# Kernel tuning notes

Measured on AMD Instinct MI355X. Metric: run time of the kernel, lower is better.

Reference implementation:

```python
import jax, jax.numpy as jnp
import numpy as np

D = 128
H = 256


def setup_inputs() -> dict:
    key = jax.random.key(0)
    ks = jax.random.split(key, 16)
    B, T = 512, 128
    C = D + H + D  # combined = [x, h, mask]
    stdv_c = 1.0 / np.sqrt(C)
    stdv_d = 1.0 / np.sqrt(D)
    stdv_h = 1.0 / np.sqrt(H)
    u = lambda k, shape, s: jax.random.uniform(k, shape, jnp.float32, -s, s)
    return {
        "input": jax.random.normal(ks[0], (B, 4, T, D), jnp.float32),
        "X_mean": jax.random.normal(ks[1], (1, T, D), jnp.float32),
        "zl_w": u(ks[2], (H, C), stdv_c), "zl_b": u(ks[3], (H,), stdv_c),
        "rl_w": u(ks[4], (H, C), stdv_c), "rl_b": u(ks[5], (H,), stdv_c),
        "hl_w": u(ks[6], (H, C), stdv_c), "hl_b": u(ks[7], (H,), stdv_c),
        "gx_w": u(ks[8], (D, D), stdv_d), "gx_b": u(ks[9], (D,), stdv_d),
        "gh_w": u(ks[10], (H, D), stdv_d), "gh_b": u(ks[11], (H,), stdv_d),
        "fc_w": u(ks[12], (1, H), stdv_h), "fc_b": u(ks[13], (1,), stdv_h),
    }


def reference(input, X_mean, zl_w, zl_b, rl_w, rl_b, hl_w, hl_b,
              gx_w, gx_b, gh_w, gh_b, fc_w, fc_b):
    B = input.shape[0]
    # FilterLinear with identity filter: weight is masked to its diagonal
    gx_w_masked = gx_w * jnp.eye(D, dtype=gx_w.dtype)
    gx_diag = jnp.diagonal(gx_w_masked)  # elementwise equivalent

    # split channels and move time to leading axis for scan: [T, B, D]
    X = jnp.moveaxis(input[:, 0], 1, 0)
    X_last = jnp.moveaxis(input[:, 1], 1, 0)
    Mask = jnp.moveaxis(input[:, 2], 1, 0)
    Delta = jnp.moveaxis(input[:, 3], 1, 0)
    Xm = jnp.moveaxis(X_mean, 1, 0)  # [T, 1, D], broadcasts over batch

    h0 = jnp.zeros((B, H), jnp.float32)

    def step(h, inp):
        x, x_last, x_mean, m, d = inp
        delta_x = jnp.exp(-jax.nn.relu(d * gx_diag + gx_b))          # [B, D]
        delta_h = jnp.exp(-jax.nn.relu(d @ gh_w.T + gh_b))           # [B, H]
        x = m * x + (1 - m) * (delta_x * x_last + (1 - delta_x) * x_mean)
        h = delta_h * h
        combined = jnp.concatenate([x, h, m], axis=1)                # [B, D+H+D]
        z = jax.nn.sigmoid(combined @ zl_w.T + zl_b)
        r = jax.nn.sigmoid(combined @ rl_w.T + rl_b)
        combined_r = jnp.concatenate([x, r * h, m], axis=1)
        h_tilde = jnp.tanh(combined_r @ hl_w.T + hl_b)
        h = (1 - z) * h + z * h_tilde
        return h, h

    _, hs = jax.lax.scan(step, h0, (X, X_last, Xm, Mask, Delta))     # [T, B, H]
    outputs = jnp.moveaxis(hs, 0, 1)                                 # [B, T, H]
    # num_class == 2, output_last == False: binary head on all steps
    out = jax.nn.sigmoid(outputs @ fc_w.T + fc_b)                    # [B, T, 1]
    return out.astype(jnp.float32)
```

## Files before the change

kernel.cpp:

```cpp
#include <hip/hip_runtime.h>
#include <hip/hip_bf16.h>
#include <cstdint>

typedef unsigned int u32;
typedef unsigned short u16;
typedef __attribute__((ext_vector_type(8))) short bf16x8;
typedef __attribute__((ext_vector_type(4))) float f32x4;

#define TT 128
#define BB 512
#define DD 128
#define HH 256
#define CC 512

#define HDA_OFF 32768
#define PA_OFF  34816

#define BAR() do { asm volatile("s_waitcnt lgkmcnt(0)" ::: "memory"); \
                   __builtin_amdgcn_s_barrier(); \
                   asm volatile("" ::: "memory"); } while(0)

__device__ __forceinline__ u16 f2bf(float f){
  u32 u = __builtin_bit_cast(u32, f);
  u += 0x7FFFu + ((u >> 16) & 1u);
  return (u16)(u >> 16);
}
__device__ __forceinline__ float bflo(u32 w){ return __builtin_bit_cast(float, w << 16); }
__device__ __forceinline__ float bfhi(u32 w){ return __builtin_bit_cast(float, w & 0xFFFF0000u); }
__device__ __forceinline__ float bf1(u16 w){ return __builtin_bit_cast(float, ((u32)w) << 16); }
__device__ __forceinline__ float sigm(float x){ return 1.f / (1.f + __expf(-x)); }
__device__ __forceinline__ float tanh_fast(float x){
  float t = __expf(-2.f * fabsf(x));
  float r = (1.f - t) / (1.f + t);
  return copysignf(r, x);
}

__global__ __launch_bounds__(256) void prep_weights(
    const float* __restrict__ zl_w, const float* __restrict__ rl_w,
    const float* __restrict__ hl_w, const float* __restrict__ gh_w,
    const float* __restrict__ gx_w,
    u32* __restrict__ zlB, u32* __restrict__ rlB, u32* __restrict__ hlF,
    u32* __restrict__ Bpre, u32* __restrict__ ghF, float* __restrict__ gxd){
  int gid = blockIdx.x * 256 + threadIdx.x;
  if (gid < 32768){
    int d   = gid & 3;
    int l   = (gid >> 2) & 63;
    int kt  = (gid >> 8) & 7;
    int ntg = (gid >> 11) & 15;
    int nn  = 16*ntg + (l & 15);
    int kk  = 32*kt + 8*(l >> 4) + 2*d;
    int c0 = 128 + kk;
    zlB[gid] = (u32)f2bf(zl_w[nn*CC + c0]) | ((u32)f2bf(zl_w[nn*CC + c0 + 1]) << 16);
    rlB[gid] = (u32)f2bf(rl_w[nn*CC + c0]) | ((u32)f2bf(rl_w[nn*CC + c0 + 1]) << 16);
    hlF[gid] = (u32)f2bf(hl_w[nn*CC + c0]) | ((u32)f2bf(hl_w[nn*CC + c0 + 1]) << 16);
  }
  #pragma unroll
  for (int q = 0; q < 2; ++q){
    int id = q*65536 + gid;
    if (id < 98304){
      int d2 = id & 3;
      int l  = (id >> 2) & 63;
      int kt = (id >> 8) & 7;
      int nt = id >> 11;
      int g  = nt >> 4;
      int nc = (nt & 15)*16 + (l & 15);
      int k  = 32*kt + 8*(l >> 4) + 2*d2;
      int sc = (k < 128) ? k : k + 256;
      const float* W = (g == 0) ? zl_w : ((g == 1) ? rl_w : hl_w);
      Bpre[id] = (u32)f2bf(W[nc*CC + sc]) | ((u32)f2bf(W[nc*CC + sc + 1]) << 16);
    }
  }
  if (gid < 16384){
    int d2 = gid & 3;
    int l  = (gid >> 2) & 63;
    int kt = (gid >> 8) & 3;
    int nt = gid >> 10;
    int nc = nt*16 + (l & 15);
    int k  = 32*kt + 8*(l >> 4) + 2*d2;
    ghF[gid] = (u32)f2bf(gh_w[nc*DD + k]) | ((u32)f2bf(gh_w[nc*DD + k + 1]) << 16);
  }
  if (gid < 128) gxd[gid] = gx_w[gid*DD + gid];
}

__global__ __launch_bounds__(512, 2) void precompute_mfma(
    const float* __restrict__ input, const float* __restrict__ xmean,
    const float* __restrict__ gxd, const float* __restrict__ gx_b,
    const float* __restrict__ zl_b, const float* __restrict__ rl_b,
    const float* __restrict__ hl_b, const float* __restrict__ gh_b,
    const u32* __restrict__ Bpre, const u32* __restrict__ ghF,
    u32* __restrict__ zrp, float* __restrict__ hpre, float* __restrict__ dh){
  __shared__ __align__(16) u16 A1[4][8][64][8];
  __shared__ __align__(16) u16 A2[4][4][64][8];
  const int tid = threadIdx.x;
  const int r0 = blockIdx.x * 64;
  const int t  = r0 >> 9;
  const int b0 = r0 & 511;
  {
    int row = tid >> 3, dsg = tid & 7, d0 = dsg * 16;
    int b = b0 + row;
    const size_t ib = ((size_t)b * 4 * TT + t) * DD;
    int mt = row >> 4;
    #pragma unroll
    for (int gg = 0; gg < 2; ++gg){
      int db = d0 + 8*gg;
      float xv[8], lv[8], mv[8], dv[8], xm[8], gd[8], gb[8];
      #pragma unroll
      for (int q = 0; q < 2; ++q){
        *(float4*)&xv[q*4] = *(const float4*)&input[ib + 0*TT*DD + db + q*4];
        *(float4*)&lv[q*4] = *(const float4*)&input[ib + 1*TT*DD + db + q*4];
        *(float4*)&mv[q*4] = *(const float4*)&input[ib + 2*TT*DD + db + q*4];
        *(float4*)&dv[q*4] = *(const float4*)&input[ib + 3*TT*DD + db + q*4];
        *(float4*)&xm[q*4] = *(const float4*)&xmean[t*DD + db + q*4];
        *(float4*)&gd[q*4] = *(const float4*)&gxd[db + q*4];
        *(float4*)&gb[q*4] = *(const float4*)&gx_b[db + q*4];
      }
      union { u16 s[8]; bf16x8 v; } pe, pm, pd;
      #pragma unroll
      for (int j = 0; j < 8; ++j){
        float dxv = __expf(-fmaxf(dv[j]*gd[j] + gb[j], 0.f));
        float xe  = mv[j]*xv[j] + (1.f - mv[j])*(dxv*lv[j] + (1.f - dxv)*xm[j]);
        pe.s[j] = f2bf(xe);
        pm.s[j] = f2bf(mv[j]);
        pd.s[j] = f2bf(dv[j]);
      }
      int kt1 = db >> 5;
      int l1  = (row & 15) + 16*((db >> 3) & 3);
      *(bf16x8*)&A1[mt][kt1][l1][0]     = pe.v;
      *(bf16x8*)&A1[mt][4 + kt1][l1][0] = pm.v;
      *(bf16x8*)&A2[mt][kt1][l1][0]     = pd.v;
    }
  }
  __syncthreads();
  const int l = tid & 63, w = tid >> 6;
  const int wm = w >> 2, wn = w & 3;
  const int rowl = 4 * (l >> 4), coll = l & 15;
  f32x4 acc[2][12];
  #pragma unroll
  for (int m = 0; m < 2; ++m)
    #pragma unroll
    for (int i = 0; i < 12; ++i) acc[m][i] = (f32x4){0.f,0.f,0.f,0.f};
  #pragma unroll
  for (int kt = 0; kt < 8; ++kt){
    bf16x8 a0 = *(const bf16x8*)&A1[wm*2 + 0][kt][l][0];
    bf16x8 a1 = *(const bf16x8*)&A1[wm*2 + 1][kt][l][0];
    #pragma unroll
    for (int i = 0; i < 12; ++i){
      int nt = 4*i + wn;
      bf16x8 bf = *(const bf16x8*)(Bpre + ((nt*8 + kt)*64 + l)*4);
      acc[0][i] = __builtin_amdgcn_mfma_f32_16x16x32_bf16(a0, bf, acc[0][i], 0, 0, 0);
      acc[1][i] = __builtin_amdgcn_mfma_f32_16x16x32_bf16(a1, bf, acc[1][i], 0, 0, 0);
    }
  }
  #pragma unroll
  for (int m = 0; m < 2; ++m){
    int grow = r0 + wm*32 + m*16 + rowl;
    #pragma unroll
    for (int i = 0; i < 4; ++i){
      int lc = (4*i + wn)*16 + coll;
      float bz = zl_b[lc], br = rl_b[lc];
      #pragma unroll
      for (int rg = 0; rg < 4; ++rg){
        u32 pk = (u32)f2bf(acc[m][i][rg] + bz) | ((u32)f2bf(acc[m][i+4][rg] + br) << 16);
        zrp[(size_t)(grow + rg)*HH + lc] = pk;
      }
    }
    #pragma unroll
    for (int i = 8; i < 12; ++i){
      int lc = (4*(i-8) + wn)*16 + coll;
      float bh = hl_b[lc];
      #pragma unroll
      for (int rg = 0; rg < 4; ++rg)
        hpre[(size_t)(grow + rg)*HH + lc] = acc[m][i][rg] + bh;
    }
  }
  f32x4 ac2[2][4];
  #pragma unroll
  for (int m = 0; m < 2; ++m)
    #pragma unroll
    for (int i = 0; i < 4; ++i) ac2[m][i] = (f32x4){0.f,0.f,0.f,0.f};
  #pragma unroll
  for (int kt = 0; kt < 4; ++kt){
    bf16x8 a0 = *(const bf16x8*)&A2[wm*2 + 0][kt][l][0];
    bf16x8 a1 = *(const bf16x8*)&A2[wm*2 + 1][kt][l][0];
    #pragma unroll
    for (int i = 0; i < 4; ++i){
      int nt = wn*4 + i;
      bf16x8 bf = *(const bf16x8*)(ghF + ((nt*4 + kt)*64 + l)*4);
      ac2[0][i] = __builtin_amdgcn_mfma_f32_16x16x32_bf16(a0, bf, ac2[0][i], 0, 0, 0);
      ac2[1][i] = __builtin_amdgcn_mfma_f32_16x16x32_bf16(a1, bf, ac2[1][i], 0, 0, 0);
    }
  }
  #pragma unroll
  for (int m = 0; m < 2; ++m){
    int grow = r0 + wm*32 + m*16 + rowl;
    #pragma unroll
    for (int i = 0; i < 4; ++i){
      int lc = (wn*4 + i)*16 + coll;
      float bias = gh_b[lc];
      #pragma unroll
      for (int rg = 0; rg < 4; ++rg)
        dh[(size_t)(grow + rg)*HH + lc] = __expf(-fmaxf(ac2[m][i][rg] + bias, 0.f));
    }
  }
}

__global__ __launch_bounds__(512, 2) void recurrent_mfma(
    const u32* __restrict__ zrp, const float* __restrict__ hpre,
    const float* __restrict__ dh,
    const u32* __restrict__ zlB, const u32* __restrict__ rlB,
    const u32* __restrict__ hlF, u16* __restrict__ hout){
  __shared__ u32 smem[36864];
  const int tid = threadIdx.x;
  const int l = tid & 63, w = tid >> 6;
  const int b0 = blockIdx.x * 16;
  const int rowb = 4 * (l >> 4);
  const int col0 = 32*w + (l & 15);

  #pragma unroll
  for (int i = 0; i < 64; ++i) smem[i*512 + tid] = hlF[i*512 + tid];
  #pragma unroll
  for (int i = 0; i < 4; ++i) smem[HDA_OFF + i*512 + tid] = 0;

  bf16x8 zb[2][8], rb[2][8];
  #pragma unroll
  for (int nt = 0; nt < 2; ++nt){
    #pragma unroll
    for (int kt = 0; kt < 8; ++kt){
      int off = (((w*2 + nt)*8 + kt)*64 + l)*4;
      zb[nt][kt] = *(const bf16x8*)(zlB + off);
      rb[nt][kt] = *(const bf16x8*)(rlB + off);
    }
  }
  __syncthreads();

  int scb[2];
  #pragma unroll
  for (int nt = 0; nt < 2; ++nt)
    scb[nt] = w*512 + (2*nt + ((l >> 3) & 1))*128 + rowb*8 + (l & 7);

  float hdreg[2][4] = {{0.f,0.f,0.f,0.f},{0.f,0.f,0.f,0.f}};
  float zreg[2][4];

  u16* pa16 = (u16*)(smem + PA_OFF);
  u16* hd16 = (u16*)(smem + HDA_OFF);

  u32 zrC[2][4]; float phC[2][4], pdC[2][4];
  #pragma unroll
  for (int nt = 0; nt < 2; ++nt){
    #pragma unroll
    for (int jr = 0; jr < 4; ++jr){
      size_t o  = ((size_t)b0 + rowb + jr)*HH + col0 + 16*nt;
      size_t o2 = ((size_t)BB + b0 + rowb + jr)*HH + col0 + 16*nt;
      zrC[nt][jr] = zrp[o];
      phC[nt][jr] = hpre[o];
      pdC[nt][jr] = dh[o2];
    }
  }

  for (int t = 0; t < TT; ++t){
    u32 zrN[2][4]; float phN[2][4], pdN[2][4];
    {
      int tn  = (t < TT-1) ? t+1 : TT-1;
      int tn2 = (t < TT-2) ? t+2 : TT-1;
      #pragma unroll
      for (int nt = 0; nt < 2; ++nt){
        #pragma unroll
        for (int jr = 0; jr < 4; ++jr){
          size_t o  = ((size_t)tn *BB + b0 + rowb + jr)*HH + col0 + 16*nt;
          size_t o2 = ((size_t)tn2*BB + b0 + rowb + jr)*HH + col0 + 16*nt;
          zrN[nt][jr] = zrp[o];
          phN[nt][jr] = hpre[o];
          pdN[nt][jr] = dh[o2];
        }
      }
    }
    f32x4 cz[2] = {{0.f,0.f,0.f,0.f},{0.f,0.f,0.f,0.f}};
    f32x4 cr[2] = {{0.f,0.f,0.f,0.f},{0.f,0.f,0.f,0.f}};
    #pragma unroll
    for (int kt = 0; kt < 8; ++kt){
      bf16x8 a = *(const bf16x8*)(smem + HDA_OFF + kt*256 + l*4);
      cz[0] = __builtin_amdgcn_mfma_f32_16x16x32_bf16(a, zb[0][kt], cz[0], 0, 0, 0);
      cz[1] = __builtin_amdgcn_mfma_f32_16x16x32_bf16(a, zb[1][kt], cz[1], 0, 0, 0);
      cr[0] = __builtin_amdgcn_mfma_f32_16x16x32_bf16(a, rb[0][kt], cr[0], 0, 0, 0);
      cr[1] = __builtin_amdgcn_mfma_f32_16x16x32_bf16(a, rb[1][kt], cr[1], 0, 0, 0);
    }
    #pragma unroll
    for (int nt = 0; nt < 2; ++nt){
      #pragma unroll
      for (int jr = 0; jr < 4; ++jr){
        float zv = sigm(bflo(zrC[nt][jr]) + cz[nt][jr]);
        float rv = sigm(bfhi(zrC[nt][jr]) + cr[nt][jr]);
        zreg[nt][jr] = zv;
        pa16[scb[nt] + jr*8] = f2bf(rv * hdreg[nt][jr]);
      }
    }
    BAR();
    f32x4 ch[2] = {{0.f,0.f,0.f,0.f},{0.f,0.f,0.f,0.f}};
    #pragma unroll
    for (int kt = 0; kt < 8; ++kt){
      bf16x8 a  = *(const bf16x8*)(smem + PA_OFF + kt*256 + l*4);
      bf16x8 bh0 = *(const bf16x8*)(smem + ((2*w+0)*8 + kt)*256 + l*4);
      bf16x8 bh1 = *(const bf16x8*)(smem + ((2*w+1)*8 + kt)*256 + l*4);
      ch[0] = __builtin_amdgcn_mfma_f32_16x16x32_bf16(a, bh0, ch[0], 0, 0, 0);
      ch[1] = __builtin_amdgcn_mfma_f32_16x16x32_bf16(a, bh1, ch[1], 0, 0, 0);
    }
    #pragma unroll
    for (int nt = 0; nt < 2; ++nt){
      #pragma unroll
      for (int jr = 0; jr < 4; ++jr){
        float ht = tanh_fast(phC[nt][jr] + ch[nt][jr]);
        float hd = hdreg[nt][jr];
        float zv = zreg[nt][jr];
        float hn = (1.f - zv)*hd + zv*ht;
        size_t o = ((size_t)t*BB + b0 + rowb + jr)*HH + col0 + 16*nt;
        hout[o] = f2bf(hn);
        float hdn = pdC[nt][jr] * hn;
        hdreg[nt][jr] = hdn;
        hd16[scb[nt] + jr*8] = f2bf(hdn);
      }
    }
    BAR();
    #pragma unroll
    for (int nt = 0; nt < 2; ++nt){
      #pragma unroll
      for (int jr = 0; jr < 4; ++jr){
        zrC[nt][jr] = zrN[nt][jr];
        phC[nt][jr] = phN[nt][jr];
        pdC[nt][jr] = pdN[nt][jr];
      }
    }
  }
}

__global__ __launch_bounds__(256) void head(const u16* __restrict__ hout,
    const float* __restrict__ fc_w, const float* __restrict__ fc_b,
    float* __restrict__ out){
  int w = threadIdx.x >> 6, lane = threadIdx.x & 63;
  int rr = blockIdx.x * 4 + w;
  const ushort4 hv = *(const ushort4*)&hout[(size_t)rr*HH + lane*4];
  const float4 fw = *(const float4*)&fc_w[lane*4];
  float s = bf1(hv.x)*fw.x + bf1(hv.y)*fw.y + bf1(hv.z)*fw.z + bf1(hv.w)*fw.w;
  #pragma unroll
  for (int o = 32; o >= 1; o >>= 1) s += __shfl_xor(s, o, 64);
  if (lane == 0){
    int t = rr >> 9, b = rr & 511;
    out[b*TT + t] = sigm(s + fc_b[0]);
  }
}

extern "C" void kernel_launch(void* const* d_in, const int* in_sizes, int n_in,
                              void* d_out, int out_size, void* d_ws, size_t ws_size,
                              hipStream_t stream) {
  const float* input = (const float*)d_in[0];
  const float* xmean = (const float*)d_in[1];
  const float* zl_w  = (const float*)d_in[2];
  const float* zl_b  = (const float*)d_in[3];
  const float* rl_w  = (const float*)d_in[4];
  const float* rl_b  = (const float*)d_in[5];
  const float* hl_w  = (const float*)d_in[6];
  const float* hl_b  = (const float*)d_in[7];
  const float* gx_w  = (const float*)d_in[8];
  const float* gx_b  = (const float*)d_in[9];
  const float* gh_w  = (const float*)d_in[10];
  const float* gh_b  = (const float*)d_in[11];
  const float* fc_w  = (const float*)d_in[12];
  const float* fc_b  = (const float*)d_in[13];
  float* out = (float*)d_out;

  const size_t S = (size_t)TT * BB * HH;
  u32*   zrp  = (u32*)d_ws;
  float* hpre = (float*)(zrp + S);
  float* dhp  = hpre + S;
  u16*   hout = (u16*)(dhp + S);
  u32*   zlB  = (u32*)(hout + S);
  u32*   rlB  = zlB + 32768;
  u32*   hlF  = rlB + 32768;
  u32*   Bpre = hlF + 32768;
  u32*   ghF  = Bpre + 98304;
  float* gxd  = (float*)(ghF + 16384);

  prep_weights<<<256, 256, 0, stream>>>(zl_w, rl_w, hl_w, gh_w, gx_w,
                                        zlB, rlB, hlF, Bpre, ghF, gxd);
  precompute_mfma<<<1024, 512, 0, stream>>>(input, xmean, gxd, gx_b,
                                            zl_b, rl_b, hl_b, gh_b,
                                            Bpre, ghF,
                                            zrp, hpre, dhp);
  recurrent_mfma<<<32, 512, 0, stream>>>(zrp, hpre, dhp, zlB, rlB, hlF, hout);
  head<<<16384, 256, 0, stream>>>(hout, fc_w, fc_b, out);
}
```

Baseline: 753.8 us.

## Pack hpre and decay into bf16 and split recurrent tiles into two 8-row groups

The precompute kernel now writes the candidate pre-activation and the hidden decay factor together as one packed bf16 pair per element, replacing two fp32 streams. This cuts global traffic and the per-step loads in the recurrent kernel. The recurrent kernel now splits each 16-row batch tile into two groups of 8 real rows, each padded with duplicated rows and using its own LDS buffers. Every step issues twice as many independent MFMA chains to hide latency, only valid lanes write outputs, and the duplicated rows add redundant matrix work. Storing the candidate pre-activation and the decay in bf16 also lowers their precision.

```diff
diff --git a/kernel.cpp b/kernel.cpp
--- a/kernel.cpp
+++ b/kernel.cpp
@@ -13,8 +13,10 @@
 #define HH 256
 #define CC 512
 
-#define HDA_OFF 32768
-#define PA_OFF  34816
+#define HD0O 32768
+#define HD1O 34816
+#define P0O  36864
+#define P1O  38912
 
 #define BAR() do { asm volatile("s_waitcnt lgkmcnt(0)" ::: "memory"); \
                    __builtin_amdgcn_s_barrier(); \
@@ -88,7 +90,7 @@
     const float* __restrict__ zl_b, const float* __restrict__ rl_b,
     const float* __restrict__ hl_b, const float* __restrict__ gh_b,
     const u32* __restrict__ Bpre, const u32* __restrict__ ghF,
-    u32* __restrict__ zrp, float* __restrict__ hpre, float* __restrict__ dh){
+    u32* __restrict__ zrp, u32* __restrict__ hpd){
   __shared__ __align__(16) u16 A1[4][8][64][8];
   __shared__ __align__(16) u16 A2[4][4][64][8];
   const int tid = threadIdx.x;
@@ -151,28 +153,6 @@
       acc[1][i] = __builtin_amdgcn_mfma_f32_16x16x32_bf16(a1, bf, acc[1][i], 0, 0, 0);
     }
   }
-  #pragma unroll
-  for (int m = 0; m < 2; ++m){
-    int grow = r0 + wm*32 + m*16 + rowl;
-    #pragma unroll
-    for (int i = 0; i < 4; ++i){
-      int lc = (4*i + wn)*16 + coll;
-      float bz = zl_b[lc], br = rl_b[lc];
-      #pragma unroll
-      for (int rg = 0; rg < 4; ++rg){
-        u32 pk = (u32)f2bf(acc[m][i][rg] + bz) | ((u32)f2bf(acc[m][i+4][rg] + br) << 16);
-        zrp[(size_t)(grow + rg)*HH + lc] = pk;
-      }
-    }
-    #pragma unroll
-    for (int i = 8; i < 12; ++i){
-      int lc = (4*(i-8) + wn)*16 + coll;
-      float bh = hl_b[lc];
-      #pragma unroll
-      for (int rg = 0; rg < 4; ++rg)
-        hpre[(size_t)(grow + rg)*HH + lc] = acc[m][i][rg] + bh;
-    }
-  }
   f32x4 ac2[2][4];
   #pragma unroll
   for (int m = 0; m < 2; ++m)
@@ -184,7 +164,7 @@
     bf16x8 a1 = *(const bf16x8*)&A2[wm*2 + 1][kt][l][0];
     #pragma unroll
     for (int i = 0; i < 4; ++i){
-      int nt = wn*4 + i;
+      int nt = 4*i + wn;
       bf16x8 bf = *(const bf16x8*)(ghF + ((nt*4 + kt)*64 + l)*4);
       ac2[0][i] = __builtin_amdgcn_mfma_f32_16x16x32_bf16(a0, bf, ac2[0][i], 0, 0, 0);
       ac2[1][i] = __builtin_amdgcn_mfma_f32_16x16x32_bf16(a1, bf, ac2[1][i], 0, 0, 0);
@@ -195,31 +175,36 @@
     int grow = r0 + wm*32 + m*16 + rowl;
     #pragma unroll
     for (int i = 0; i < 4; ++i){
-      int lc = (wn*4 + i)*16 + coll;
-      float bias = gh_b[lc];
-      #pragma unroll
-      for (int rg = 0; rg < 4; ++rg)
-        dh[(size_t)(grow + rg)*HH + lc] = __expf(-fmaxf(ac2[m][i][rg] + bias, 0.f));
+      int lc = (4*i + wn)*16 + coll;
+      float bz = zl_b[lc], br = rl_b[lc], bh = hl_b[lc], bg = gh_b[lc];
+      #pragma unroll
+      for (int rg = 0; rg < 4; ++rg){
+        size_t o = (size_t)(grow + rg)*HH + lc;
+        zrp[o] = (u32)f2bf(acc[m][i][rg] + bz) | ((u32)f2bf(acc[m][i+4][rg] + br) << 16);
+        float dhv = __expf(-fmaxf(ac2[m][i][rg] + bg, 0.f));
+        hpd[o] = (u32)f2bf(acc[m][i+8][rg] + bh) | ((u32)f2bf(dhv) << 16);
+      }
     }
   }
 }
 
 __global__ __launch_bounds__(512, 2) void recurrent_mfma(
-    const u32* __restrict__ zrp, const float* __restrict__ hpre,
-    const float* __restrict__ dh,
+    const u32* __restrict__ zrp, const u32* __restrict__ hpd,
     const u32* __restrict__ zlB, const u32* __restrict__ rlB,
     const u32* __restrict__ hlF, u16* __restrict__ hout){
-  __shared__ u32 smem[36864];
+  __shared__ u32 smem[40960];
   const int tid = threadIdx.x;
   const int l = tid & 63, w = tid >> 6;
   const int b0 = blockIdx.x * 16;
   const int rowb = 4 * (l >> 4);
   const int col0 = 32*w + (l & 15);
+  const int rcl  = (rowb) & 7;
+  const bool valid = (rowb < 8);
 
   #pragma unroll
   for (int i = 0; i < 64; ++i) smem[i*512 + tid] = hlF[i*512 + tid];
   #pragma unroll
-  for (int i = 0; i < 4; ++i) smem[HDA_OFF + i*512 + tid] = 0;
+  for (int i = 0; i < 8; ++i) smem[HD0O + i*512 + tid] = 0;
 
   bf16x8 zb[2][8], rb[2][8];
   #pragma unroll
@@ -238,97 +223,119 @@
   for (int nt = 0; nt < 2; ++nt)
     scb[nt] = w*512 + (2*nt + ((l >> 3) & 1))*128 + rowb*8 + (l & 7);
 
-  float hdreg[2][4] = {{0.f,0.f,0.f,0.f},{0.f,0.f,0.f,0.f}};
-  float zreg[2][4];
-
-  u16* pa16 = (u16*)(smem + PA_OFF);
-  u16* hd16 = (u16*)(smem + HDA_OFF);
-
-  u32 zrC[2][4]; float phC[2][4], pdC[2][4];
-  #pragma unroll
-  for (int nt = 0; nt < 2; ++nt){
-    #pragma unroll
-    for (int jr = 0; jr < 4; ++jr){
-      size_t o  = ((size_t)b0 + rowb + jr)*HH + col0 + 16*nt;
-      size_t o2 = ((size_t)BB + b0 + rowb + jr)*HH + col0 + 16*nt;
-      zrC[nt][jr] = zrp[o];
-      phC[nt][jr] = hpre[o];
-      pdC[nt][jr] = dh[o2];
-    }
-  }
+  float hdreg[2][2][4];
+  #pragma unroll
+  for (int g = 0; g < 2; ++g)
+    #pragma unroll
+    for (int nt = 0; nt < 2; ++nt)
+      #pragma unroll
+      for (int jr = 0; jr < 4; ++jr) hdreg[g][nt][jr] = 0.f;
+
+  u16* pa16[2] = { (u16*)(smem + P0O),  (u16*)(smem + P1O)  };
+  u16* hd16[2] = { (u16*)(smem + HD0O), (u16*)(smem + HD1O) };
+
+  u32 zrC[2][2][4], hpC[2][2][4];
+  #pragma unroll
+  for (int g = 0; g < 2; ++g)
+    #pragma unroll
+    for (int nt = 0; nt < 2; ++nt)
+      #pragma unroll
+      for (int jr = 0; jr < 4; ++jr){
+        size_t o = ((size_t)b0 + 8*g + rcl + jr)*HH + col0 + 16*nt;
+        zrC[g][nt][jr] = zrp[o];
+        hpC[g][nt][jr] = hpd[o];
+      }
 
   for (int t = 0; t < TT; ++t){
-    u32 zrN[2][4]; float phN[2][4], pdN[2][4];
+    u32 zrN[2][2][4], hpN[2][2][4];
     {
-      int tn  = (t < TT-1) ? t+1 : TT-1;
-      int tn2 = (t < TT-2) ? t+2 : TT-1;
-      #pragma unroll
-      for (int nt = 0; nt < 2; ++nt){
+      int tn = (t < TT-1) ? t+1 : TT-1;
+      #pragma unroll
+      for (int g = 0; g < 2; ++g)
+        #pragma unroll
+        for (int nt = 0; nt < 2; ++nt)
+          #pragma unroll
+          for (int jr = 0; jr < 4; ++jr){
+            size_t o = ((size_t)tn*BB + b0 + 8*g + rcl + jr)*HH + col0 + 16*nt;
+            zrN[g][nt][jr] = zrp[o];
+            hpN[g][nt][jr] = hpd[o];
+          }
+    }
+    f32x4 cz[2][2], cr[2][2];
+    #pragma unroll
+    for (int g = 0; g < 2; ++g)
+      #pragma unroll
+      for (int nt = 0; nt < 2; ++nt){ cz[g][nt] = (f32x4){0,0,0,0}; cr[g][nt] = (f32x4){0,0,0,0}; }
+    #pragma unroll
+    for (int kt = 0; kt < 8; ++kt){
+      bf16x8 a0 = *(const bf16x8*)(smem + HD0O + kt*256 + l*4);
+      bf16x8 a1 = *(const bf16x8*)(smem + HD1O + kt*256 + l*4);
+      cz[0][0] = __builtin_amdgcn_mfma_f32_16x16x32_bf16(a0, zb[0][kt], cz[0][0], 0, 0, 0);
+      cz[1][0] = __builtin_amdgcn_mfma_f32_16x16x32_bf16(a1, zb[0][kt], cz[1][0], 0, 0, 0);
+      cz[0][1] = __builtin_amdgcn_mfma_f32_16x16x32_bf16(a0, zb[1][kt], cz[0][1], 0, 0, 0);
+      cz[1][1] = __builtin_amdgcn_mfma_f32_16x16x32_bf16(a1, zb[1][kt], cz[1][1], 0, 0, 0);
+      cr[0][0] = __builtin_amdgcn_mfma_f32_16x16x32_bf16(a0, rb[0][kt], cr[0][0], 0, 0, 0);
+      cr[1][0] = __builtin_amdgcn_mfma_f32_16x16x32_bf16(a1, rb[0][kt], cr[1][0], 0, 0, 0);
+      cr[0][1] = __builtin_amdgcn_mfma_f32_16x16x32_bf16(a0, rb[1][kt], cr[0][1], 0, 0, 0);
+      cr[1][1] = __builtin_amdgcn_mfma_f32_16x16x32_bf16(a1, rb[1][kt], cr[1][1], 0, 0, 0);
+    }
+    float zreg[2][2][4];
+    #pragma unroll
+    for (int g = 0; g < 2; ++g)
+      #pragma unroll
+      for (int nt = 0; nt < 2; ++nt)
         #pragma unroll
         for (int jr = 0; jr < 4; ++jr){
-          size_t o  = ((size_t)tn *BB + b0 + rowb + jr)*HH + col0 + 16*nt;
-          size_t o2 = ((size_t)tn2*BB + b0 + rowb + jr)*HH + col0 + 16*nt;
-          zrN[nt][jr] = zrp[o];
-          phN[nt][jr] = hpre[o];
-          pdN[nt][jr] = dh[o2];
+          float zv = sigm(bflo(zrC[g][nt][jr]) + cz[g][nt][jr]);
+          float rv = sigm(bfhi(zrC[g][nt][jr]) + cr[g][nt][jr]);
+          zreg[g][nt][jr] = zv;
+          pa16[g][scb[nt] + jr*8] = f2bf(rv * hdreg[g][nt][jr]);
         }
-      }
-    }
-    f32x4 cz[2] = {{0.f,0.f,0.f,0.f},{0.f,0.f,0.f,0.f}};
-    f32x4 cr[2] = {{0.f,0.f,0.f,0.f},{0.f,0.f,0.f,0.f}};
+    BAR();
+    f32x4 ch[2][2];
+    #pragma unroll
+    for (int g = 0; g < 2; ++g)
+      #pragma unroll
+      for (int nt = 0; nt < 2; ++nt) ch[g][nt] = (f32x4){0,0,0,0};
     #pragma unroll
     for (int kt = 0; kt < 8; ++kt){
-      bf16x8 a = *(const bf16x8*)(smem + HDA_OFF + kt*256 + l*4);
-      cz[0] = __builtin_amdgcn_mfma_f32_16x16x32_bf16(a, zb[0][kt], cz[0], 0, 0, 0);
-      cz[1] = __builtin_amdgcn_mfma_f32_16x16x32_bf16(a, zb[1][kt], cz[1], 0, 0, 0);
-      cr[0] = __builtin_amdgcn_mfma_f32_16x16x32_bf16(a, rb[0][kt], cr[0], 0, 0, 0);
-      cr[1] = __builtin_amdgcn_mfma_f32_16x16x32_bf16(a, rb[1][kt], cr[1], 0, 0, 0);
-    }
-    #pragma unroll
-    for (int nt = 0; nt < 2; ++nt){
-      #pragma unroll
-      for (int jr = 0; jr < 4; ++jr){
-        float zv = sigm(bflo(zrC[nt][jr]) + cz[nt][jr]);
-        float rv = sigm(bfhi(zrC[nt][jr]) + cr[nt][jr]);
-        zreg[nt][jr] = zv;
-        pa16[scb[nt] + jr*8] = f2bf(rv * hdreg[nt][jr]);
-      }
-    }
-    BAR();
-    f32x4 ch[2] = {{0.f,0.f,0.f,0.f},{0.f,0.f,0.f,0.f}};
-    #pragma unroll
-    for (int kt = 0; kt < 8; ++kt){
-      bf16x8 a  = *(const bf16x8*)(smem + PA_OFF + kt*256 + l*4);
+      bf16x8 p0 = *(const bf16x8*)(smem + P0O + kt*256 + l*4);
+      bf16x8 p1 = *(const bf16x8*)(smem + P1O + kt*256 + l*4);
       bf16x8 bh0 = *(const bf16x8*)(smem + ((2*w+0)*8 + kt)*256 + l*4);
       bf16x8 bh1 = *(const bf16x8*)(smem + ((2*w+1)*8 + kt)*256 + l*4);
-      ch[0] = __builtin_amdgcn_mfma_f32_16x16x32_bf16(a, bh0, ch[0], 0, 0, 0);
-      ch[1] = __builtin_amdgcn_mfma_f32_16x16x32_bf16(a, bh1, ch[1], 0, 0, 0);
-    }
-    #pragma unroll
-    for (int nt = 0; nt < 2; ++nt){
-      #pragma unroll
-      for (int jr = 0; jr < 4; ++jr){
-        float ht = tanh_fast(phC[nt][jr] + ch[nt][jr]);
-        float hd = hdreg[nt][jr];
-        float zv = zreg[nt][jr];
-        float hn = (1.f - zv)*hd + zv*ht;
-        size_t o = ((size_t)t*BB + b0 + rowb + jr)*HH + col0 + 16*nt;
-        hout[o] = f2bf(hn);
-        float hdn = pdC[nt][jr] * hn;
-        hdreg[nt][jr] = hdn;
-        hd16[scb[nt] + jr*8] = f2bf(hdn);
-      }
-    }
+      ch[0][0] = __builtin_amdgcn_mfma_f32_16x16x32_bf16(p0, bh0, ch[0][0], 0, 0, 0);
+      ch[1][0] = __builtin_amdgcn_mfma_f32_16x16x32_bf16(p1, bh0, ch[1][0], 0, 0, 0);
+      ch[0][1] = __builtin_amdgcn_mfma_f32_16x16x32_bf16(p0, bh1, ch[0][1], 0, 0, 0);
+      ch[1][1] = __builtin_amdgcn_mfma_f32_16x16x32_bf16(p1, bh1, ch[1][1], 0, 0, 0);
+    }
+    #pragma unroll
+    for (int g = 0; g < 2; ++g)
+      #pragma unroll
+      for (int nt = 0; nt < 2; ++nt)
+        #pragma unroll
+        for (int jr = 0; jr < 4; ++jr){
+          float ht = tanh_fast(bflo(hpC[g][nt][jr]) + ch[g][nt][jr]);
+          float hd = hdreg[g][nt][jr];
+          float zv = zreg[g][nt][jr];
+          float hn = (1.f - zv)*hd + zv*ht;
+          if (valid){
+            size_t o = ((size_t)t*BB + b0 + 8*g + rowb + jr)*HH + col0 + 16*nt;
+            hout[o] = f2bf(hn);
+          }
+          float hdn = bfhi(hpN[g][nt][jr]) * hn;
+          hdreg[g][nt][jr] = hdn;
+          hd16[g][scb[nt] + jr*8] = f2bf(hdn);
+        }
     BAR();
     #pragma unroll
-    for (int nt = 0; nt < 2; ++nt){
-      #pragma unroll
-      for (int jr = 0; jr < 4; ++jr){
-        zrC[nt][jr] = zrN[nt][jr];
-        phC[nt][jr] = phN[nt][jr];
-        pdC[nt][jr] = pdN[nt][jr];
-      }
-    }
+    for (int g = 0; g < 2; ++g)
+      #pragma unroll
+      for (int nt = 0; nt < 2; ++nt)
+        #pragma unroll
+        for (int jr = 0; jr < 4; ++jr){
+          zrC[g][nt][jr] = zrN[g][nt][jr];
+          hpC[g][nt][jr] = hpN[g][nt][jr];
+        }
   }
 }
 
@@ -369,9 +376,8 @@
 
   const size_t S = (size_t)TT * BB * HH;
   u32*   zrp  = (u32*)d_ws;
-  float* hpre = (float*)(zrp + S);
-  float* dhp  = hpre + S;
-  u16*   hout = (u16*)(dhp + S);
+  u32*   hpd  = zrp + S;
+  u16*   hout = (u16*)(hpd + S);
   u32*   zlB  = (u32*)(hout + S);
   u32*   rlB  = zlB + 32768;
   u32*   hlF  = rlB + 32768;
@@ -383,8 +389,7 @@
                                         zlB, rlB, hlF, Bpre, ghF, gxd);
   precompute_mfma<<<1024, 512, 0, stream>>>(input, xmean, gxd, gx_b,
                                             zl_b, rl_b, hl_b, gh_b,
-                                            Bpre, ghF,
-                                            zrp, hpre, dhp);
-  recurrent_mfma<<<32, 512, 0, stream>>>(zrp, hpre, dhp, zlB, rlB, hlF, hout);
+                                            Bpre, ghF, zrp, hpd);
+  recurrent_mfma<<<32, 512, 0, stream>>>(zrp, hpd, zlB, rlB, hlF, hout);
   head<<<16384, 256, 0, stream>>>(hout, fc_w, fc_b, out);
 }
```

Measured after the change: 1.437 ms. +90.6%, slower.
